# Kernel tuning notes

Hardware: AMD Instinct MI355X
Metric: run time of the kernel (lower is better)

## Reference

```python
import jax, jax.numpy as jnp
import numpy as np

LATENT = 1024
RED = 4            # reduce_proj
GROUPS = 16
K = 3              # kernel_size
PAD = 1
REGIONS = 36
CPG = LATENT // GROUPS   # channels per group (in and out), = 64
NEG = 0.1                # LeakyReLU slope


def l2norm(x, axis=-1):
    # faithful to lavse l2norm: x / sqrt(sum(x^2)) with no eps
    return x / jnp.sqrt(jnp.sum(x * x, axis=axis, keepdims=True))


def leaky(x):
    return jnp.where(x > 0, x, NEG * x)


def setup_inputs() -> dict:
    key = jax.random.key(0)
    ks = jax.random.split(key, 7)
    Bi, Bc, T = 128, 32, 50
    img_embed = jax.random.normal(ks[0], (Bi, REGIONS, LATENT), jnp.float32)
    cap_embed = jax.random.normal(ks[1], (Bc, T, LATENT), jnp.float32)
    lens = jax.random.randint(ks[2], (Bc,), 1, T + 1)  # word counts in [1, T]
    qdim = LATENT // RED
    s1 = 1.0 / np.sqrt(LATENT)
    red_w = jax.random.uniform(ks[3], (LATENT, qdim), jnp.float32, -s1, s1)
    red_b = jax.random.uniform(ks[4], (qdim,), jnp.float32, -s1, s1)
    nw = LATENT * CPG * K  # out_channels * (in_channels // groups) * kernel_size
    s2 = 1.0 / np.sqrt(qdim)
    proj_w = jax.random.uniform(ks[5], (qdim, nw), jnp.float32, -s2, s2)
    proj_b = jax.random.uniform(ks[6], (nw,), jnp.float32, -s2, s2)
    return dict(img_embed=img_embed, cap_embed=cap_embed, lens=lens,
                red_w=red_w, red_b=red_b, proj_w=proj_w, proj_b=proj_b)


def reference(img_embed, cap_embed, lens, red_w, red_b, proj_w, proj_b):
    Bi = img_embed.shape[0]
    Bc, T, C = cap_embed.shape
    # masked mean over the first n_words of each caption -> (Bc, C)
    mask = (jnp.arange(T)[None, :] < lens[:, None]).astype(cap_embed.dtype)
    cap_repr = jnp.sum(cap_embed * mask[:, :, None], axis=1) / lens[:, None].astype(cap_embed.dtype)
    cap_act = leaky(cap_repr)                       # 'cap' gate, (Bc, C)
    # dynamic depthwise-grouped conv weights from reduced query
    q = cap_repr @ red_w + red_b                    # (Bc, qdim)
    w = (q @ proj_w + proj_b).reshape(Bc, LATENT, CPG, K)
    w = jax.nn.softmax(w, axis=-1)                  # weightnorm='softmax' over kernel dim
    w = w.reshape(Bc, GROUPS, CPG, CPG, K)          # (Bc, g, out/g, in/g, K)
    # grouped conv1d over 36 regions, padding=1
    img = img_embed.transpose(0, 2, 1)              # (Bi, C, L)
    imgp = jnp.pad(img, ((0, 0), (0, 0), (PAD, PAD)))
    shif = jnp.stack([imgp[:, :, k:k + REGIONS] for k in range(K)], axis=-1)  # (Bi, C, L, K)
    shif = shif.reshape(Bi, GROUPS, CPG, REGIONS, K)
    out = jnp.einsum('bgilk,ngoik->nbgol', shif, w).reshape(Bc, Bi, LATENT, REGIONS)
    out = leaky(out)
    # (x * cap).mean(-1) == x.mean(-1) * cap since cap broadcasts over positions
    img_vec = l2norm(jnp.mean(out, axis=-1) * cap_act[:, None, :])  # (Bc, Bi, C)
    cap_vec = l2norm(cap_repr)                                      # (Bc, C)
    sims = jnp.einsum('nbc,nc->bn', img_vec, cap_vec)               # (Bi, Bc)
    return sims
```

## Files before the change

### kernel.cpp

```cpp
#include <hip/hip_runtime.h>
#include <math.h>

#define LATENT 1024
#define QDIM 256
#define NW 196608
#define BI 128
#define BC 32
#define TT 50
#define REGIONS 36
#define NGROUPS 16
#define CPG 64
#define NEG 0.1f

typedef __attribute__((ext_vector_type(8))) short short8;
typedef __attribute__((ext_vector_type(16))) float f32x16;

__device__ __forceinline__ float leakyf(float x){ return x > 0.f ? x : NEG * x; }

__device__ __forceinline__ unsigned short f2bf(float x){
    union { float f; unsigned int u; } v; v.f = x;
    unsigned int r = v.u + 0x7FFFu + ((v.u >> 16) & 1u);
    return (unsigned short)(r >> 16);
}

__global__ __launch_bounds__(256) void cap_mean_kernel(
    const float* __restrict__ cap_embed, const int* __restrict__ lens,
    float* __restrict__ cap_repr, float* __restrict__ cap_act,
    float* __restrict__ norm_capr)
{
    const int n = blockIdx.x;
    const int len = lens[n];
    const float invl = 1.f / (float)len;
    const int c4 = threadIdx.x;
    const float* base = cap_embed + (size_t)n * TT * LATENT + c4 * 4;
    float4 s = {0.f, 0.f, 0.f, 0.f};
    for (int t = 0; t < len; ++t) {
        const float4 v = *reinterpret_cast<const float4*>(base + (size_t)t * LATENT);
        s.x += v.x; s.y += v.y; s.z += v.z; s.w += v.w;
    }
    float4 m = {s.x * invl, s.y * invl, s.z * invl, s.w * invl};
    *reinterpret_cast<float4*>(cap_repr + n * LATENT + c4 * 4) = m;
    const float sc = 1.f / 36.f;
    float4 a = {leakyf(m.x) * sc, leakyf(m.y) * sc, leakyf(m.z) * sc, leakyf(m.w) * sc};
    *reinterpret_cast<float4*>(cap_act + n * LATENT + c4 * 4) = a;
    float ss = m.x*m.x + m.y*m.y + m.z*m.z + m.w*m.w;
    #pragma unroll
    for (int off = 32; off; off >>= 1) ss += __shfl_xor(ss, off);
    __shared__ float red4[4];
    if ((threadIdx.x & 63) == 0) red4[threadIdx.x >> 6] = ss;
    __syncthreads();
    if (threadIdx.x == 0) norm_capr[n] = sqrtf(red4[0] + red4[1] + red4[2] + red4[3]);
}

__global__ __launch_bounds__(256) void q_kernel(
    const float* __restrict__ cap_repr, const float* __restrict__ red_w,
    const float* __restrict__ red_b, unsigned short* __restrict__ qbfF)
{
    const int cg = blockIdx.x, n = blockIdx.y;
    const int col = threadIdx.x & 31, ks = threadIdx.x >> 5;
    const float* cr = cap_repr + n * LATENT;
    float p = 0.f;
    const int r0 = ks * 128;
    for (int r = r0; r < r0 + 128; ++r)
        p = fmaf(cr[r], red_w[(size_t)r * QDIM + cg * 32 + col], p);
    __shared__ float part[256];
    part[threadIdx.x] = p;
    __syncthreads();
    if (threadIdx.x < 32) {
        float s = red_b[cg * 32 + col];
        #pragma unroll
        for (int k = 0; k < 8; ++k) s += part[k * 32 + col];
        const int r = cg * 32 + col;
        const int elem = (r >> 4) * 512 + ((r >> 3) & 1) * 256 + n * 8 + (r & 7);
        qbfF[elem] = f2bf(s);
    }
}

__global__ __launch_bounds__(384) void wgen9_kernel(
    const unsigned short* __restrict__ qbfF, const float* __restrict__ proj_w,
    const float* __restrict__ proj_b, unsigned short* __restrict__ Wp2F)
{
    __shared__ float L[192 * 33];
    __shared__ float pbs[192];
    const int tid = threadIdx.x;
    const int g = blockIdx.x >> 6, o = blockIdx.x & 63;
    const int colbase = (g * 64 + o) * 192;
    const int wv = tid >> 6, lane = tid & 63;
    const int lrow = lane & 31, khalf = lane >> 5;

    if (tid < 192) pbs[tid] = proj_b[colbase + tid];

    short8 qfr[16];
    {
        const unsigned short* qp = qbfF + (size_t)lane * 8;
        #pragma unroll
        for (int s = 0; s < 16; ++s)
            qfr[s] = *reinterpret_cast<const short8*>(qp + s * 512);
    }

    const float* pw0 = proj_w + (size_t)(khalf * 8) * NW + colbase + wv * 32 + lrow;

    float a[8], b[8];
    #pragma unroll
    for (int j = 0; j < 8; ++j) a[j] = pw0[(size_t)j * NW];

    f32x16 acc = {};
    #pragma unroll
    for (int s = 0; s < 16; ++s) {
        if (s < 15) {
            const float* pwn = pw0 + (size_t)((s + 1) * 16) * NW;
            #pragma unroll
            for (int j = 0; j < 8; ++j) b[j] = pwn[(size_t)j * NW];
        }
        unsigned short u[8];
        #pragma unroll
        for (int j = 0; j < 8; ++j) u[j] = f2bf(a[j]);
        const short8 af = *reinterpret_cast<const short8*>(u);
        acc = __builtin_amdgcn_mfma_f32_32x32x16_bf16(af, qfr[s], acc, 0, 0, 0);
        #pragma unroll
        for (int j = 0; j < 8; ++j) a[j] = b[j];
    }

    __syncthreads();
    #pragma unroll
    for (int reg = 0; reg < 16; ++reg) {
        const int rit = (reg & 3) + 8 * (reg >> 2) + 4 * khalf;
        const int c = wv * 32 + rit;
        L[c * 33 + lrow] = acc[reg] + pbs[c];
    }
    __syncthreads();

    const int nt = o >> 5, lrow_o = o & 31;
    for (int idx = tid; idx < 2048; idx += 384) {
        const int n = idx & 31, i = idx >> 5;
        const int c = i * 3;
        const float x0 = L[c * 33 + n], x1 = L[(c+1)*33 + n], x2 = L[(c+2)*33 + n];
        const float m = fmaxf(fmaxf(x0, x1), x2);
        const float e0 = expf(x0 - m), e1 = expf(x1 - m), e2 = expf(x2 - m);
        const float inv = 1.f / (e0 + e1 + e2);
        const int ks = i >> 4, kh = (i >> 3) & 1, j = i & 7;
        const size_t base = (size_t)(n * 16 + g) * 12288
                          + (size_t)(nt * 4 + ks) * 512
                          + kh * 256 + lrow_o * 8 + j;
        Wp2F[base]        = f2bf(e0 * inv);
        Wp2F[base + 4096] = f2bf(e1 * inv);
        Wp2F[base + 8192] = f2bf(e2 * inv);
    }
}

__global__ __launch_bounds__(576, 3) void conv5_kernel(
    const float* __restrict__ img_embed, const unsigned short* __restrict__ Wp2F,
    const float* __restrict__ cap_repr, const float* __restrict__ cap_act,
    float* __restrict__ part_dot, float* __restrict__ part_ss)
{
    const int g = blockIdx.x, bt = blockIdx.y, nq = blockIdx.z;
    const int b0 = bt * 8;
    __shared__ int4 BsmV[3072];
    char* BsmRaw = (char*)BsmV;
    __shared__ float Sw[2][9][2][64];
    const int tid = threadIdx.x;
    const int wv = tid >> 6, lane = tid & 63;
    const int lrow = lane & 31, khalf = lane >> 5;
    const int ioff = khalf * 16;

    const float* imgG = img_embed + (size_t)b0 * 36 * 1024 + g * 64;
    for (int idx = tid; idx < 2304; idx += 576) {
        const int row_img = idx >> 3, ch = idx & 7;
        const int bbs = row_img / 36;
        const int l = row_img - bbs * 36;
        const float* src = imgG + (size_t)row_img * 1024 + ch * 8;
        const float4 u = *reinterpret_cast<const float4*>(src);
        const float4 v = *reinterpret_cast<const float4*>(src + 4);
        unsigned short r8[8];
        r8[0]=f2bf(u.x); r8[1]=f2bf(u.y); r8[2]=f2bf(u.z); r8[3]=f2bf(u.w);
        r8[4]=f2bf(v.x); r8[5]=f2bf(v.y); r8[6]=f2bf(v.z); r8[7]=f2bf(v.w);
        const int arow = bbs * 38 + l + 1;
        const int byte = (arow * 128 + ch * 16) ^ ((arow & 7) << 4);
        *reinterpret_cast<int4*>(BsmRaw + byte) = *reinterpret_cast<const int4*>(r8);
    }
    if (tid < 128) {
        const int rr = tid >> 3, ch = tid & 7;
        const int arow = (rr >> 1) * 38 + (rr & 1) * 37;
        const int byte = (arow * 128 + ch * 16) ^ ((arow & 7) << 4);
        int4 z; z.x = 0; z.y = 0; z.z = 0; z.w = 0;
        *reinterpret_cast<int4*>(BsmRaw + byte) = z;
    }
    __syncthreads();

    const int rg = wv * 32 + lrow;
    const int bbr = rg / 36;
    const int abase = bbr * 38 + (rg - bbr * 36);
    short8 afr[3][4];
    #pragma unroll
    for (int k = 0; k < 3; ++k)
        #pragma unroll
        for (int ks = 0; ks < 4; ++ks) {
            const int arow = abase + k;
            const int byte = (arow * 128 + ks * 32 + ioff) ^ ((arow & 7) << 4);
            afr[k][ks] = *reinterpret_cast<const short8*>(BsmRaw + byte);
        }
    const int rbase = wv * 32;
    const int bfirst = rbase / 36;
    const int bsplit = (bfirst + 1) * 36 - rbase;
    __syncthreads();

    const int n0 = nq * 16;
    int4 st0, st1, st2;
    {
        const unsigned short* WF = Wp2F + (size_t)(n0 * 16 + g) * 12288;
        st0 = *reinterpret_cast<const int4*>(WF + (size_t)tid * 8);
        st1 = *reinterpret_cast<const int4*>(WF + (size_t)(tid + 576) * 8);
        if (tid < 384) st2 = *reinterpret_cast<const int4*>(WF + (size_t)(tid + 1152) * 8);
        *reinterpret_cast<int4*>(BsmRaw + (size_t)tid * 16) = st0;
        *reinterpret_cast<int4*>(BsmRaw + (size_t)(tid + 576) * 16) = st1;
        if (tid < 384) *reinterpret_cast<int4*>(BsmRaw + (size_t)(tid + 1152) * 16) = st2;
    }
    __syncthreads();

    for (int ni = 0; ni < 16; ++ni) {
        const int n = n0 + ni;
        char* Bcur = BsmRaw + (size_t)(ni & 1) * 24576;
        char* Bnxt = BsmRaw + (size_t)((ni + 1) & 1) * 24576;

        if (ni < 15) {
            const unsigned short* WF = Wp2F + (size_t)((n + 1) * 16 + g) * 12288;
            st0 = *reinterpret_cast<const int4*>(WF + (size_t)tid * 8);
            st1 = *reinterpret_cast<const int4*>(WF + (size_t)(tid + 576) * 8);
            if (tid < 384) st2 = *reinterpret_cast<const int4*>(WF + (size_t)(tid + 1152) * 8);
        }

        f32x16 acc0 = {}, acc1 = {};
        #pragma unroll
        for (int k = 0; k < 3; ++k) {
            #pragma unroll
            for (int ks = 0; ks < 4; ++ks) {
                const char* fb = Bcur + k * 8192 + ks * 1024 + (size_t)lane * 16;
                const short8 bf0 = *reinterpret_cast<const short8*>(fb);
                const short8 bf1 = *reinterpret_cast<const short8*>(fb + 4096);
                acc0 = __builtin_amdgcn_mfma_f32_32x32x16_bf16(afr[k][ks], bf0, acc0, 0, 0, 0);
                acc1 = __builtin_amdgcn_mfma_f32_32x32x16_bf16(afr[k][ks], bf1, acc1, 0, 0, 0);
            }
        }

        if (ni < 15) {
            *reinterpret_cast<int4*>(Bnxt + (size_t)tid * 16) = st0;
            *reinterpret_cast<int4*>(Bnxt + (size_t)(tid + 576) * 16) = st1;
            if (tid < 384) *reinterpret_cast<int4*>(Bnxt + (size_t)(tid + 1152) * 16) = st2;
        }

        float s0A = 0.f, s0B = 0.f, s1A = 0.f, s1B = 0.f;
        #pragma unroll
        for (int reg = 0; reg < 16; ++reg) {
            const int rit = (reg & 3) + 8 * (reg >> 2) + 4 * khalf;
            const float v0 = leakyf(acc0[reg]);
            const float v1 = leakyf(acc1[reg]);
            if (rit >= bsplit) { s0B += v0; s1B += v1; }
            else               { s0A += v0; s1A += v1; }
        }
        s0A += __shfl_xor(s0A, 32); s0B += __shfl_xor(s0B, 32);
        s1A += __shfl_xor(s1A, 32); s1B += __shfl_xor(s1B, 32);
        const int q = ni & 1;
        if (khalf == 0) {
            Sw[q][wv][0][lrow]      = s0A;
            Sw[q][wv][0][32 + lrow] = s1A;
            if (bsplit < 32) {
                Sw[q][wv][1][lrow]      = s0B;
                Sw[q][wv][1][32 + lrow] = s1B;
            }
        }
        __syncthreads();

        if (tid < 128) {
            const int b = tid >> 4, j = tid & 15;
            const float4 ca4 = *reinterpret_cast<const float4*>(&cap_act [n * LATENT + g * CPG + j * 4]);
            const float4 cr4 = *reinterpret_cast<const float4*>(&cap_repr[n * LATENT + g * CPG + j * 4]);
            const float cav[4] = {ca4.x, ca4.y, ca4.z, ca4.w};
            const float crv[4] = {cr4.x, cr4.y, cr4.z, cr4.w};
            float d = 0.f, ss = 0.f;
            #pragma unroll
            for (int u = 0; u < 4; ++u) {
                const int o = j * 4 + u;
                const float S = (b == 0)
                    ? Sw[q][0][0][o] + Sw[q][1][0][o]
                    : Sw[q][b][1][o] + Sw[q][b + 1][0][o];
                const float tmp = S * cav[u];
                d = fmaf(tmp, crv[u], d);
                ss = fmaf(tmp, tmp, ss);
            }
            #pragma unroll
            for (int off = 1; off <= 8; off <<= 1) {
                d += __shfl_xor(d, off);
                ss += __shfl_xor(ss, off);
            }
            if (j == 0) {
                part_dot[((size_t)n * BI + b0 + b) * NGROUPS + g] = d;
                part_ss [((size_t)n * BI + b0 + b) * NGROUPS + g] = ss;
            }
        }
    }
}

__global__ __launch_bounds__(256) void final_kernel(
    const float* __restrict__ part_dot, const float* __restrict__ part_ss,
    const float* __restrict__ norm_capr, float* __restrict__ out)
{
    const int idx = blockIdx.x * 256 + threadIdx.x;
    const int n = idx & 31;
    const int b = idx >> 5;
    const size_t base = ((size_t)n * BI + b) * NGROUPS;
    float d = 0.f, s = 0.f;
    #pragma unroll
    for (int g = 0; g < NGROUPS; ++g) { d += part_dot[base + g]; s += part_ss[base + g]; }
    out[b * BC + n] = d / (sqrtf(s) * norm_capr[n]);
}

extern "C" void kernel_launch(void* const* d_in, const int* in_sizes, int n_in,
                              void* d_out, int out_size, void* d_ws, size_t ws_size,
                              hipStream_t stream) {
    const float* img_embed = (const float*)d_in[0];
    const float* cap_embed = (const float*)d_in[1];
    const int*   lens      = (const int*)  d_in[2];
    const float* red_w     = (const float*)d_in[3];
    const float* red_b     = (const float*)d_in[4];
    const float* proj_w    = (const float*)d_in[5];
    const float* proj_b    = (const float*)d_in[6];
    float* out = (float*)d_out;

    char* ws = (char*)d_ws;
    unsigned short* Wp2F   = (unsigned short*)(ws);
    float* cap_repr  = (float*)(ws + 22020096);
    float* cap_act   = (float*)(ws + 22151168);
    unsigned short* qbfF = (unsigned short*)(ws + 22282240);
    float* norm_capr = (float*)(ws + 22315008);
    float* part_dot  = (float*)(ws + 22315520);
    float* part_ss   = (float*)(ws + 22577664);

    hipLaunchKernelGGL(cap_mean_kernel, dim3(BC), dim3(256), 0, stream,
                       cap_embed, lens, cap_repr, cap_act, norm_capr);
    hipLaunchKernelGGL(q_kernel, dim3(8, BC), dim3(256), 0, stream,
                       cap_repr, red_w, red_b, qbfF);
    hipLaunchKernelGGL(wgen9_kernel, dim3(1024), dim3(384), 0, stream,
                       qbfF, proj_w, proj_b, Wp2F);
    hipLaunchKernelGGL(conv5_kernel, dim3(NGROUPS, 16, 2), dim3(576), 0, stream,
                       img_embed, Wp2F, cap_repr, cap_act, part_dot, part_ss);
    hipLaunchKernelGGL(final_kernel, dim3(16), dim3(256), 0, stream,
                       part_dot, part_ss, norm_capr, out);
}
```

Before: 180.8 us.

## Widen weight-generation blocks to 768 columns with three accumulators per wave

The weight-generation GEMM now has each block cover 768 output columns (4 output channels) using 8 waves, and each wave runs three independent MFMA accumulators over 96 columns instead of one over 32. The grid shrinks from 1024 blocks to 256, so the bf16 query fragments are loaded fewer times and each wave has more independent loads and MFMAs in flight. In exchange, register pressure and LDS use per block (about 99KB) go up. Only 256 blocks remain, which may underfill the GPU's compute units and lower occupancy in this memory-bound stage. The LDS row padding of 33 is dropped to 32, which can cause bank conflicts in the softmax reads.

Measured after the change: 176.6 us. 1.02x faster.

```diff
diff --git a/kernel.cpp b/kernel.cpp
--- a/kernel.cpp
+++ b/kernel.cpp
@@ -76,19 +76,19 @@
     }
 }
 
-__global__ __launch_bounds__(384) void wgen9_kernel(
+__global__ __launch_bounds__(512, 2) void wgen10_kernel(
     const unsigned short* __restrict__ qbfF, const float* __restrict__ proj_w,
     const float* __restrict__ proj_b, unsigned short* __restrict__ Wp2F)
 {
-    __shared__ float L[192 * 33];
-    __shared__ float pbs[192];
+    __shared__ float L[768 * 32];
+    __shared__ float pbs[768];
     const int tid = threadIdx.x;
-    const int g = blockIdx.x >> 6, o = blockIdx.x & 63;
-    const int colbase = (g * 64 + o) * 192;
+    const int bx = blockIdx.x;
+    const int colbase = bx * 768;
     const int wv = tid >> 6, lane = tid & 63;
     const int lrow = lane & 31, khalf = lane >> 5;
 
-    if (tid < 192) pbs[tid] = proj_b[colbase + tid];
+    for (int i = tid; i < 768; i += 512) pbs[i] = proj_b[colbase + i];
 
     short8 qfr[16];
     {
@@ -98,47 +98,66 @@
             qfr[s] = *reinterpret_cast<const short8*>(qp + s * 512);
     }
 
-    const float* pw0 = proj_w + (size_t)(khalf * 8) * NW + colbase + wv * 32 + lrow;
-
-    float a[8], b[8];
-    #pragma unroll
-    for (int j = 0; j < 8; ++j) a[j] = pw0[(size_t)j * NW];
-
-    f32x16 acc = {};
+    const float* pw0 = proj_w + (size_t)(khalf * 8) * NW + colbase + wv * 96 + lrow;
+    const float* pw1 = pw0 + 32;
+    const float* pw2 = pw0 + 64;
+
+    float a0[8], a1[8], a2[8], b0[8], b1[8], b2[8];
+    #pragma unroll
+    for (int j = 0; j < 8; ++j) {
+        a0[j] = pw0[(size_t)j * NW];
+        a1[j] = pw1[(size_t)j * NW];
+        a2[j] = pw2[(size_t)j * NW];
+    }
+
+    f32x16 acc0 = {}, acc1 = {}, acc2 = {};
     #pragma unroll
     for (int s = 0; s < 16; ++s) {
         if (s < 15) {
-            const float* pwn = pw0 + (size_t)((s + 1) * 16) * NW;
+            const size_t roff = (size_t)((s + 1) * 16) * NW;
             #pragma unroll
-            for (int j = 0; j < 8; ++j) b[j] = pwn[(size_t)j * NW];
-        }
-        unsigned short u[8];
-        #pragma unroll
-        for (int j = 0; j < 8; ++j) u[j] = f2bf(a[j]);
-        const short8 af = *reinterpret_cast<const short8*>(u);
-        acc = __builtin_amdgcn_mfma_f32_32x32x16_bf16(af, qfr[s], acc, 0, 0, 0);
-        #pragma unroll
-        for (int j = 0; j < 8; ++j) a[j] = b[j];
+            for (int j = 0; j < 8; ++j) {
+                b0[j] = pw0[roff + (size_t)j * NW];
+                b1[j] = pw1[roff + (size_t)j * NW];
+                b2[j] = pw2[roff + (size_t)j * NW];
+            }
+        }
+        unsigned short u0[8], u1[8], u2[8];
+        #pragma unroll
+        for (int j = 0; j < 8; ++j) {
+            u0[j] = f2bf(a0[j]); u1[j] = f2bf(a1[j]); u2[j] = f2bf(a2[j]);
+        }
+        acc0 = __builtin_amdgcn_mfma_f32_32x32x16_bf16(*reinterpret_cast<const short8*>(u0), qfr[s], acc0, 0, 0, 0);
+        acc1 = __builtin_amdgcn_mfma_f32_32x32x16_bf16(*reinterpret_cast<const short8*>(u1), qfr[s], acc1, 0, 0, 0);
+        acc2 = __builtin_amdgcn_mfma_f32_32x32x16_bf16(*reinterpret_cast<const short8*>(u2), qfr[s], acc2, 0, 0, 0);
+        #pragma unroll
+        for (int j = 0; j < 8; ++j) { a0[j] = b0[j]; a1[j] = b1[j]; a2[j] = b2[j]; }
     }
 
     __syncthreads();
     #pragma unroll
     for (int reg = 0; reg < 16; ++reg) {
         const int rit = (reg & 3) + 8 * (reg >> 2) + 4 * khalf;
-        const int c = wv * 32 + rit;
-        L[c * 33 + lrow] = acc[reg] + pbs[c];
-    }
-    __syncthreads();
-
-    const int nt = o >> 5, lrow_o = o & 31;
-    for (int idx = tid; idx < 2048; idx += 384) {
+        const int c = wv * 96 + rit;
+        L[c * 32 + lrow]        = acc0[reg] + pbs[c];
+        L[(c + 32) * 32 + lrow] = acc1[reg] + pbs[c + 32];
+        L[(c + 64) * 32 + lrow] = acc2[reg] + pbs[c + 64];
+    }
+    __syncthreads();
+
+    const int g = bx >> 4;
+    const int obase = (bx & 15) * 4;
+    for (int idx = tid; idx < 8192; idx += 512) {
         const int n = idx & 31, i = idx >> 5;
         const int c = i * 3;
-        const float x0 = L[c * 33 + n], x1 = L[(c+1)*33 + n], x2 = L[(c+2)*33 + n];
+        const float x0 = L[c * 32 + n], x1 = L[(c+1)*32 + n], x2 = L[(c+2)*32 + n];
         const float m = fmaxf(fmaxf(x0, x1), x2);
         const float e0 = expf(x0 - m), e1 = expf(x1 - m), e2 = expf(x2 - m);
         const float inv = 1.f / (e0 + e1 + e2);
-        const int ks = i >> 4, kh = (i >> 3) & 1, j = i & 7;
+        const int o = obase + (i >> 6);
+        const int ii = i & 63;
+        const int nt = o >> 5, lrow_o = o & 31;
+        const int ks = ii >> 4, kh = (ii >> 3) & 1, j = ii & 7;
         const size_t base = (size_t)(n * 16 + g) * 12288
                           + (size_t)(nt * 4 + ks) * 512
                           + kh * 256 + lrow_o * 8 + j;
@@ -339,7 +358,7 @@
                        cap_embed, lens, cap_repr, cap_act, norm_capr);
     hipLaunchKernelGGL(q_kernel, dim3(8, BC), dim3(256), 0, stream,
                        cap_repr, red_w, red_b, qbfF);
-    hipLaunchKernelGGL(wgen9_kernel, dim3(1024), dim3(384), 0, stream,
+    hipLaunchKernelGGL(wgen10_kernel, dim3(256), dim3(512), 0, stream,
                        qbfF, proj_w, proj_b, Wp2F);
     hipLaunchKernelGGL(conv5_kernel, dim3(NGROUPS, 16, 2), dim3(576), 0, stream,
                        img_embed, Wp2F, cap_repr, cap_act, part_dot, part_ss);
```

## Split weight generation into float4-staged MFMA GEMM and separate softmax kernel

Applied to the files above, without the earlier changes.

The weight-generation kernel now loads proj_w with float4 vector reads, converts it to bf16, stages it through shared memory and runs two MFMA accumulators per wave over 256 columns per block. The softmax moves into its own kernel that reads fp32 logits from a new global buffer. The goal is better coalescing and throughput on the large proj_w read. The cost is an extra ~25MB fp32 global round trip, an additional launch, and more syncthreads per k-step.

Measured after the change: 199.1 us. 1.1x slower.

```diff
diff --git a/kernel.cpp b/kernel.cpp
--- a/kernel.cpp
+++ b/kernel.cpp
@@ -15,6 +15,8 @@
 typedef __attribute__((ext_vector_type(8))) short short8;
 typedef __attribute__((ext_vector_type(16))) float f32x16;
 
+#define EL(v,c) ((c)==0?(v).x:(c)==1?(v).y:(c)==2?(v).z:(v).w)
+
 __device__ __forceinline__ float leakyf(float x){ return x > 0.f ? x : NEG * x; }
 
 __device__ __forceinline__ unsigned short f2bf(float x){
@@ -76,69 +78,94 @@
     }
 }
 
-__global__ __launch_bounds__(384) void wgen9_kernel(
+__global__ __launch_bounds__(256) void wgen11_kernel(
     const unsigned short* __restrict__ qbfF, const float* __restrict__ proj_w,
-    const float* __restrict__ proj_b, unsigned short* __restrict__ Wp2F)
-{
-    __shared__ float L[192 * 33];
-    __shared__ float pbs[192];
+    const float* __restrict__ proj_b, float* __restrict__ Lg)
+{
+    __shared__ unsigned short Bsm[256 * 36];
+    __shared__ float pbs[256];
     const int tid = threadIdx.x;
-    const int g = blockIdx.x >> 6, o = blockIdx.x & 63;
-    const int colbase = (g * 64 + o) * 192;
+    const int colbase = blockIdx.x * 256;
     const int wv = tid >> 6, lane = tid & 63;
     const int lrow = lane & 31, khalf = lane >> 5;
 
-    if (tid < 192) pbs[tid] = proj_b[colbase + tid];
+    pbs[tid] = proj_b[colbase + tid];
 
     short8 qfr[16];
     {
         const unsigned short* qp = qbfF + (size_t)lane * 8;
         #pragma unroll
-        for (int s = 0; s < 16; ++s)
-            qfr[s] = *reinterpret_cast<const short8*>(qp + s * 512);
-    }
-
-    const float* pw0 = proj_w + (size_t)(khalf * 8) * NW + colbase + wv * 32 + lrow;
-
-    float a[8], b[8];
-    #pragma unroll
-    for (int j = 0; j < 8; ++j) a[j] = pw0[(size_t)j * NW];
-
-    f32x16 acc = {};
-    #pragma unroll
-    for (int s = 0; s < 16; ++s) {
-        if (s < 15) {
-            const float* pwn = pw0 + (size_t)((s + 1) * 16) * NW;
-            #pragma unroll
-            for (int j = 0; j < 8; ++j) b[j] = pwn[(size_t)j * NW];
-        }
-        unsigned short u[8];
-        #pragma unroll
-        for (int j = 0; j < 8; ++j) u[j] = f2bf(a[j]);
-        const short8 af = *reinterpret_cast<const short8*>(u);
-        acc = __builtin_amdgcn_mfma_f32_32x32x16_bf16(af, qfr[s], acc, 0, 0, 0);
-        #pragma unroll
-        for (int j = 0; j < 8; ++j) a[j] = b[j];
-    }
-
-    __syncthreads();
+        for (int s = 0; s < 16; ++s) qfr[s] = *reinterpret_cast<const short8*>(qp + s * 512);
+    }
+
+    const int cg = tid & 63, rq = tid >> 6;
+    const float* src0 = proj_w + (size_t)(rq * 8) * NW + colbase + cg * 4;
+
+    float4 st[8], nx[8];
+    #pragma unroll
+    for (int j = 0; j < 8; ++j)
+        st[j] = *reinterpret_cast<const float4*>(src0 + (size_t)j * NW);
+
+    f32x16 acc0 = {}, acc1 = {};
+    #pragma unroll
+    for (int s = 0; s < 8; ++s) {
+        __syncthreads();
+        #pragma unroll
+        for (int cc = 0; cc < 4; ++cc) {
+            unsigned short pk[8];
+            #pragma unroll
+            for (int j = 0; j < 8; ++j) pk[j] = f2bf(EL(st[j], cc));
+            *reinterpret_cast<short8*>((char*)Bsm + (cg * 4 + cc) * 72 + rq * 16) =
+                *reinterpret_cast<const short8*>(pk);
+        }
+        __syncthreads();
+        if (s < 7) {
+            const float* srcn = src0 + (size_t)((s + 1) * 32) * NW;
+            #pragma unroll
+            for (int j = 0; j < 8; ++j)
+                nx[j] = *reinterpret_cast<const float4*>(srcn + (size_t)j * NW);
+        }
+        #pragma unroll
+        for (int kc = 0; kc < 2; ++kc) {
+            const short8 a0 = *reinterpret_cast<const short8*>(
+                (char*)Bsm + (wv * 64 + lrow) * 72 + kc * 32 + khalf * 16);
+            const short8 a1 = *reinterpret_cast<const short8*>(
+                (char*)Bsm + (wv * 64 + 32 + lrow) * 72 + kc * 32 + khalf * 16);
+            acc0 = __builtin_amdgcn_mfma_f32_32x32x16_bf16(a0, qfr[s * 2 + kc], acc0, 0, 0, 0);
+            acc1 = __builtin_amdgcn_mfma_f32_32x32x16_bf16(a1, qfr[s * 2 + kc], acc1, 0, 0, 0);
+        }
+        if (s < 7) {
+            #pragma unroll
+            for (int j = 0; j < 8; ++j) st[j] = nx[j];
+        }
+    }
+
     #pragma unroll
     for (int reg = 0; reg < 16; ++reg) {
         const int rit = (reg & 3) + 8 * (reg >> 2) + 4 * khalf;
-        const int c = wv * 32 + rit;
-        L[c * 33 + lrow] = acc[reg] + pbs[c];
-    }
-    __syncthreads();
-
-    const int nt = o >> 5, lrow_o = o & 31;
-    for (int idx = tid; idx < 2048; idx += 384) {
-        const int n = idx & 31, i = idx >> 5;
-        const int c = i * 3;
-        const float x0 = L[c * 33 + n], x1 = L[(c+1)*33 + n], x2 = L[(c+2)*33 + n];
+        const int c0 = wv * 64 + rit;
+        const int c1 = c0 + 32;
+        Lg[(size_t)(colbase + c0) * 32 + lrow] = acc0[reg] + pbs[c0];
+        Lg[(size_t)(colbase + c1) * 32 + lrow] = acc1[reg] + pbs[c1];
+    }
+}
+
+__global__ __launch_bounds__(256) void softmax2_kernel(
+    const float* __restrict__ Lg, unsigned short* __restrict__ Wp2F)
+{
+    const int tripbase = blockIdx.x * 256;
+    for (int idx = threadIdx.x; idx < 8192; idx += 256) {
+        const int n = idx & 31, it = idx >> 5;
+        const int t = tripbase + it;
+        const float x0 = Lg[(size_t)(t * 3 + 0) * 32 + n];
+        const float x1 = Lg[(size_t)(t * 3 + 1) * 32 + n];
+        const float x2 = Lg[(size_t)(t * 3 + 2) * 32 + n];
         const float m = fmaxf(fmaxf(x0, x1), x2);
         const float e0 = expf(x0 - m), e1 = expf(x1 - m), e2 = expf(x2 - m);
         const float inv = 1.f / (e0 + e1 + e2);
-        const int ks = i >> 4, kh = (i >> 3) & 1, j = i & 7;
+        const int g = t >> 12, o = (t >> 6) & 63, ii = t & 63;
+        const int nt = o >> 5, lrow_o = o & 31;
+        const int ks = ii >> 4, kh = (ii >> 3) & 1, j = ii & 7;
         const size_t base = (size_t)(n * 16 + g) * 12288
                           + (size_t)(nt * 4 + ks) * 512
                           + kh * 256 + lrow_o * 8 + j;
@@ -327,20 +354,23 @@
     float* out = (float*)d_out;
 
     char* ws = (char*)d_ws;
-    unsigned short* Wp2F   = (unsigned short*)(ws);
-    float* cap_repr  = (float*)(ws + 22020096);
-    float* cap_act   = (float*)(ws + 22151168);
-    unsigned short* qbfF = (unsigned short*)(ws + 22282240);
-    float* norm_capr = (float*)(ws + 22315008);
-    float* part_dot  = (float*)(ws + 22315520);
-    float* part_ss   = (float*)(ws + 22577664);
+    unsigned short* Wp2F = (unsigned short*)(ws);
+    float* Lg        = (float*)(ws + 12582912);
+    float* cap_repr  = (float*)(ws + 37748736);
+    float* cap_act   = (float*)(ws + 37879808);
+    unsigned short* qbfF = (unsigned short*)(ws + 38010880);
+    float* norm_capr = (float*)(ws + 38027264);
+    float* part_dot  = (float*)(ws + 38027776);
+    float* part_ss   = (float*)(ws + 38289920);
 
     hipLaunchKernelGGL(cap_mean_kernel, dim3(BC), dim3(256), 0, stream,
                        cap_embed, lens, cap_repr, cap_act, norm_capr);
     hipLaunchKernelGGL(q_kernel, dim3(8, BC), dim3(256), 0, stream,
                        cap_repr, red_w, red_b, qbfF);
-    hipLaunchKernelGGL(wgen9_kernel, dim3(1024), dim3(384), 0, stream,
-                       qbfF, proj_w, proj_b, Wp2F);
+    hipLaunchKernelGGL(wgen11_kernel, dim3(768), dim3(256), 0, stream,
+                       qbfF, proj_w, proj_b, Lg);
+    hipLaunchKernelGGL(softmax2_kernel, dim3(256), dim3(256), 0, stream,
+                       Lg, Wp2F);
     hipLaunchKernelGGL(conv5_kernel, dim3(NGROUPS, 16, 2), dim3(576), 0, stream,
                        img_embed, Wp2F, cap_repr, cap_act, part_dot, part_ss);
     hipLaunchKernelGGL(final_kernel, dim3(16), dim3(256), 0, stream,
```
